# Performance work log

Measured on AMD Instinct MI355X. Metric: run time of the kernel, lower is better.

## Reference

```python
import jax, jax.numpy as jnp
import numpy as np

B, T, C = 4, 2048, 2048
N_HEAD, N_HEAD_KV = 16, 4
HEAD_DIM = C // N_HEAD
ROPE_BASE = 10000.0


def setup_inputs() -> dict:
    key = jax.random.key(0)
    ks = jax.random.split(key, 6)
    x = jax.random.normal(ks[0], (B, T, C), dtype=jnp.float32)
    # freqs_cis: (T, head_dim//2, 2) with [...,0]=cos, [...,1]=sin (true RoPE angles)
    inv_freq = 1.0 / (ROPE_BASE ** (jnp.arange(0, HEAD_DIM, 2, dtype=jnp.float32) / HEAD_DIM))
    angles = jnp.arange(T, dtype=jnp.float32)[:, None] * inv_freq[None, :]  # (T, hd//2)
    freqs_cis = jnp.stack([jnp.cos(angles), jnp.sin(angles)], axis=-1)
    s = 0.02
    Wq = jax.random.normal(ks[1], (C, C), dtype=jnp.float32) * s
    Wk = jax.random.normal(ks[2], (N_HEAD_KV * HEAD_DIM, C), dtype=jnp.float32) * s
    Wv = jax.random.normal(ks[3], (N_HEAD_KV * HEAD_DIM, C), dtype=jnp.float32) * s
    Wo = jax.random.normal(ks[4], (C, C), dtype=jnp.float32) * s
    return {"x": x, "freqs_cis": freqs_cis, "Wq": Wq, "Wk": Wk, "Wv": Wv, "Wo": Wo}


def _rotate_half(u):
    h = u.shape[-1] // 2
    return jnp.concatenate([-u[..., h:], u[..., :h]], axis=-1)


def reference(x, freqs_cis, Wq, Wk, Wv, Wo):
    b, t, c = x.shape
    hd = HEAD_DIM
    q = (x @ Wq.T).reshape(b, t, N_HEAD, hd)
    k = (x @ Wk.T).reshape(b, t, N_HEAD_KV, hd)
    v = (x @ Wv.T).reshape(b, t, N_HEAD_KV, hd)
    # external RoPE (3-dim freqs_cis): cos/sin repeated to full head_dim
    cos = freqs_cis[:t, :, 0]
    sin = freqs_cis[:t, :, 1]
    cos = jnp.concatenate([cos, cos], axis=-1)[None, :, None, :]  # (1,T,1,hd)
    sin = jnp.concatenate([sin, sin], axis=-1)[None, :, None, :]
    q = q * cos + _rotate_half(q) * sin
    k = k * cos + _rotate_half(k) * sin
    # GQA: repeat_interleave kv heads to n_head
    g = N_HEAD // N_HEAD_KV
    k = jnp.repeat(k, g, axis=2)  # (B,T,H,hd)
    v = jnp.repeat(v, g, axis=2)
    scale = 1.0 / np.sqrt(hd)
    scores = jnp.einsum('bthd,bshd->bhts', q, k) * scale  # (B,H,T,S)
    causal = jnp.tril(jnp.ones((t, t), dtype=bool))
    neg = jnp.finfo(scores.dtype).min
    scores = jnp.where(causal[None, None, :, :], scores, neg)
    attn = jax.nn.softmax(scores, axis=-1)
    out = jnp.einsum('bhts,bshd->bthd', attn, v).reshape(b, t, c)
    return out @ Wo.T
```

## Files before the change

### kernel.cpp

```cpp
#include <hip/hip_runtime.h>
#include <hip/hip_bf16.h>
#include <stdint.h>

typedef __bf16 bf16_t;
typedef __bf16 bf16x4 __attribute__((ext_vector_type(4)));
typedef __bf16 bf16x8 __attribute__((ext_vector_type(8)));
typedef float f32x4 __attribute__((ext_vector_type(4)));

__device__ __forceinline__ float fast_exp2(float x) {
#if __has_builtin(__builtin_amdgcn_exp2f)
  return __builtin_amdgcn_exp2f(x);
#else
  return exp2f(x);
#endif
}

__global__ void cvt_all(const float* __restrict__ x,  const float* __restrict__ Wq,
                        const float* __restrict__ Wk, const float* __restrict__ Wv,
                        const float* __restrict__ Wo, bf16_t* __restrict__ xb,
                        bf16_t* __restrict__ wqkv, bf16_t* __restrict__ wob) {
  const int bid = blockIdx.x, tid = threadIdx.x;
  const float* src; bf16_t* dst; int i;
  if (bid < 16384)      { src = x;  dst = xb;             i = bid * 256 + tid; }
  else if (bid < 20480) { src = Wq; dst = wqkv;           i = (bid - 16384) * 256 + tid; }
  else if (bid < 21504) { src = Wk; dst = wqkv + 4194304; i = (bid - 20480) * 256 + tid; }
  else if (bid < 22528) { src = Wv; dst = wqkv + 5242880; i = (bid - 21504) * 256 + tid; }
  else                  { src = Wo; dst = wob;            i = (bid - 22528) * 256 + tid; }
  float4 v = ((const float4*)src)[i];
  bf16x4 o = { (bf16_t)v.x, (bf16_t)v.y, (bf16_t)v.z, (bf16_t)v.w };
  *(bf16x4*)(dst + (size_t)i * 4) = o;
}

__device__ __forceinline__ void async_load16(const bf16_t* g, bf16_t* l) {
#if __has_builtin(__builtin_amdgcn_global_load_lds)
  __builtin_amdgcn_global_load_lds((const __attribute__((address_space(1))) void*)g,
                                   (__attribute__((address_space(3))) void*)l, 16, 0, 0);
#else
  *(bf16x8*)l = *(const bf16x8*)g;
#endif
}

template<bool F32OUT, bool VSPLIT>
__global__ __launch_bounds__(256) void gemm_bt(const bf16_t* __restrict__ A,
                                               const bf16_t* __restrict__ B,
                                               void* __restrict__ C,
                                               bf16_t* __restrict__ Vt,
                                               int M, int N, int K, int ldc) {
  __shared__ bf16_t Alds[128 * 64];
  __shared__ bf16_t Blds[128 * 64];
  const int tid = threadIdx.x;
  const int wave = tid >> 6, lane = tid & 63;
  const int lrow = lane & 15, quad = lane >> 4;
  const int wr = wave >> 1, wc = wave & 1;
  const int bm = blockIdx.y, bn = blockIdx.x;
  const bf16_t* Ab = A + (size_t)bm * 128 * K;
  const bf16_t* Bb = B + (size_t)bn * 128 * K;
  const int r0 = tid >> 3;
  const int c0 = ((tid & 7) ^ (r0 & 7)) << 3;
  f32x4 acc[4][4] = {};

  for (int kk = 0; kk < K; kk += 64) {
#pragma unroll
    for (int p = 0; p < 4; ++p) {
      async_load16(Ab + (size_t)(p * 32 + r0) * K + kk + c0, &Alds[(p * 256 + tid) * 8]);
      async_load16(Bb + (size_t)(p * 32 + r0) * K + kk + c0, &Blds[(p * 256 + tid) * 8]);
    }
    __syncthreads();
#pragma unroll
    for (int ks2 = 0; ks2 < 2; ++ks2) {
      const int rc = ((ks2 * 4 + quad) ^ (lrow & 7)) << 3;
      bf16x8 af[4], bfv[4];
#pragma unroll
      for (int mt = 0; mt < 4; ++mt)
        af[mt] = *(const bf16x8*)&Alds[(wr * 64 + mt * 16 + lrow) * 64 + rc];
#pragma unroll
      for (int nt = 0; nt < 4; ++nt)
        bfv[nt] = *(const bf16x8*)&Blds[(wc * 64 + nt * 16 + lrow) * 64 + rc];
#pragma unroll
      for (int mt = 0; mt < 4; ++mt)
#pragma unroll
        for (int nt = 0; nt < 4; ++nt)
          acc[mt][nt] = __builtin_amdgcn_mfma_f32_16x16x32_bf16(af[mt], bfv[nt], acc[mt][nt], 0, 0, 0);
    }
    __syncthreads();
  }

  if (VSPLIT && bn >= 20) {
#pragma unroll
    for (int mt = 0; mt < 4; ++mt)
#pragma unroll
      for (int nt = 0; nt < 4; ++nt) {
        int row = bm * 128 + wr * 64 + mt * 16 + quad * 4;
        int cv  = bn * 128 + wc * 64 + nt * 16 + lrow - 2560;
        int b = row >> 11, tl = row & 2047;
        bf16x4 o;
#pragma unroll
        for (int r = 0; r < 4; ++r) o[r] = (bf16_t)acc[mt][nt][r];
        *(bf16x4*)&Vt[((size_t)(b * 512 + cv)) * 2048 + tl] = o;
      }
    return;
  }
#pragma unroll
  for (int mt = 0; mt < 4; ++mt)
#pragma unroll
    for (int nt = 0; nt < 4; ++nt)
#pragma unroll
      for (int r = 0; r < 4; ++r) {
        int row = bm * 128 + wr * 64 + mt * 16 + quad * 4 + r;
        int col = bn * 128 + wc * 64 + nt * 16 + lrow;
        if (F32OUT) ((float*)C)[(size_t)row * ldc + col] = acc[mt][nt][r];
        else        ((bf16_t*)C)[(size_t)row * ldc + col] = (bf16_t)acc[mt][nt][r];
      }
}

__global__ void rope_kernel(bf16_t* __restrict__ X, const float* __restrict__ F,
                            int hshift, int stride) {
  int i = blockIdx.x * blockDim.x + threadIdx.x;
  int d = i & 63;
  int h = (i >> 6) & ((1 << hshift) - 1);
  int row = i >> (6 + hshift);
  int t = row & 2047;
  float c = F[t * 128 + d * 2];
  float s = F[t * 128 + d * 2 + 1];
  size_t base = (size_t)row * stride + h * 128 + d;
  float q0 = (float)X[base];
  float q1 = (float)X[base + 64];
  X[base]      = (bf16_t)(q0 * c - q1 * s);
  X[base + 64] = (bf16_t)(q1 * c + q0 * s);
}

__global__ __launch_bounds__(256, 2) void attn_kernel(const bf16_t* __restrict__ QKV,
                                                      const float* __restrict__ F,
                                                      const bf16_t* __restrict__ Vt,
                                                      bf16_t* __restrict__ O) {
  __shared__ bf16_t Ks[2][64 * 128];
  __shared__ bf16_t Vs[2][128 * 64];
  __shared__ bf16_t Ps[4 * 32 * 64];
  const int tid = threadIdx.x;
  const int wave = tid >> 6, lane = tid & 63;
  const int lrow = lane & 15, quad = lane >> 4;
  const int bh = blockIdx.y, b = bh >> 4, h = bh & 15, kvh = h >> 2;
  const size_t qoff  = ((size_t)b * 2048) * 2560 + (size_t)h * 128;
  const size_t koff  = ((size_t)b * 2048) * 2560 + 2048 + (size_t)kvh * 128;
  const size_t vtoff = ((size_t)(b * 4 + kvh) * 128) * 2048;
  const float qsc = 0.08838834764831845f * 1.44269504088896340736f;
  bf16_t* Pw = Ps + wave * (32 * 64);
  const float2* F2 = (const float2*)F;

  const int krow_l = tid >> 4;
  const int kdc    = (tid & 15) ^ (krow_l & 7);
  const int vrow_l = tid >> 3;
  const int vkc    = (tid & 7) ^ (vrow_l & 7);

  auto stage = [&](int kt, int bsel) {
    const bf16_t* Kg = QKV + koff + (size_t)(kt * 64) * 2560;
    const bf16_t* Vg = Vt + vtoff + kt * 64;
    bf16_t* Kd = &Ks[bsel][0];
    bf16_t* Vd = &Vs[bsel][0];
#pragma unroll
    for (int c4 = 0; c4 < 4; ++c4) {
      int ci = c4 * 256 + tid;
      async_load16(Kg + (size_t)(c4 * 16 + krow_l) * 2560 + kdc * 8, Kd + ci * 8);
      async_load16(Vg + (size_t)(c4 * 32 + vrow_l) * 2048 + vkc * 8, Vd + ci * 8);
    }
  };

  for (int phase = 0; phase < 2; ++phase) {
    const int qt = phase ? (15 - blockIdx.x) : blockIdx.x;
    const int qbase = qt * 128 + wave * 32;

    bf16x8 qf[2][4];
#pragma unroll
    for (int nt2 = 0; nt2 < 2; ++nt2) {
      const int t = qbase + nt2 * 16 + lrow;
      const bf16_t* qp = QKV + qoff + (size_t)t * 2560 + quad * 8;
      bf16x8 raw[4];
#pragma unroll
      for (int ks = 0; ks < 4; ++ks) raw[ks] = *(const bf16x8*)(qp + ks * 32);
#pragma unroll
      for (int ks2 = 0; ks2 < 2; ++ks2) {
        bf16x8 lo, hi;
#pragma unroll
        for (int j = 0; j < 8; ++j) {
          int d = ks2 * 32 + quad * 8 + j;
          float2 cs = F2[t * 64 + d];
          float q0 = (float)raw[ks2][j], q1 = (float)raw[ks2 + 2][j];
          lo[j] = (bf16_t)((q0 * cs.x - q1 * cs.y) * qsc);
          hi[j] = (bf16_t)((q1 * cs.x + q0 * cs.y) * qsc);
        }
        qf[nt2][ks2]     = lo;
        qf[nt2][ks2 + 2] = hi;
      }
    }

    f32x4 Oacc[2][8] = {};
    float m_r[2] = {-1.0e30f, -1.0e30f};
    float l_r[2] = {0.f, 0.f};
    const int kt_end = 2 * qt + 2;

    stage(0, 0);

    for (int kt = 0; kt < kt_end; ++kt) {
      __syncthreads();
      if (kt + 1 < kt_end) stage(kt + 1, (kt + 1) & 1);
      const bf16_t* Kb_ = &Ks[kt & 1][0];
      const bf16_t* Vb_ = &Vs[kt & 1][0];

      if (kt * 64 <= qbase + 31) {
        f32x4 S[2][4] = {};
#pragma unroll
        for (int ks = 0; ks < 4; ++ks) {
          bf16x8 kf[4];
#pragma unroll
          for (int mt = 0; mt < 4; ++mt) {
            int dc = (ks * 4 + quad) ^ (lrow & 7);
            kf[mt] = *(const bf16x8*)&Kb_[(mt * 16 + lrow) * 128 + dc * 8];
          }
          __builtin_amdgcn_s_setprio(1);
#pragma unroll
          for (int nt2 = 0; nt2 < 2; ++nt2)
#pragma unroll
            for (int mt = 0; mt < 4; ++mt)
              S[nt2][mt] = __builtin_amdgcn_mfma_f32_16x16x32_bf16(kf[mt], qf[nt2][ks], S[nt2][mt], 0, 0, 0);
          __builtin_amdgcn_s_setprio(0);
        }
        if (kt * 64 + 63 > qbase) {
#pragma unroll
          for (int nt2 = 0; nt2 < 2; ++nt2) {
            int q = qbase + nt2 * 16 + lrow;
#pragma unroll
            for (int mt = 0; mt < 4; ++mt) {
              int key0 = kt * 64 + mt * 16 + quad * 4;
#pragma unroll
              for (int r = 0; r < 4; ++r)
                if (key0 + r > q) S[nt2][mt][r] = -1.0e30f;
            }
          }
        }
        float alpha[2];
#pragma unroll
        for (int nt2 = 0; nt2 < 2; ++nt2) {
          float mx = -1.0e30f;
#pragma unroll
          for (int mt = 0; mt < 4; ++mt)
#pragma unroll
            for (int r = 0; r < 4; ++r) mx = fmaxf(mx, S[nt2][mt][r]);
          mx = fmaxf(mx, __shfl_xor(mx, 16, 64));
          mx = fmaxf(mx, __shfl_xor(mx, 32, 64));
          float mnew = fmaxf(m_r[nt2], mx);
          alpha[nt2] = fast_exp2(m_r[nt2] - mnew);
          m_r[nt2] = mnew;
          float rs = 0.f;
          const int prow = nt2 * 16 + lrow;
          const int pbase = prow * 64 + ((quad & 1) << 2);
#pragma unroll
          for (int mt = 0; mt < 4; ++mt) {
            bf16x4 pk;
#pragma unroll
            for (int r = 0; r < 4; ++r) {
              float p = fast_exp2(S[nt2][mt][r] - mnew);
              rs += p;
              pk[r] = (bf16_t)p;
            }
            int c8 = ((mt * 2 + (quad >> 1)) ^ (prow & 7)) << 3;
            *(bf16x4*)&Pw[pbase + c8] = pk;
          }
          rs += __shfl_xor(rs, 16, 64);
          rs += __shfl_xor(rs, 32, 64);
          l_r[nt2] = l_r[nt2] * alpha[nt2] + rs;
        }
        bool nz = (alpha[0] != 1.f) || (alpha[1] != 1.f);
        if (__ballot(nz) != 0ull) {
#pragma unroll
          for (int mt2 = 0; mt2 < 2; ++mt2)
#pragma unroll
            for (int r = 0; r < 4; ++r) {
              float av = __shfl(alpha[mt2], quad * 4 + r, 16);
#pragma unroll
              for (int dt = 0; dt < 8; ++dt) Oacc[mt2][dt][r] *= av;
            }
        }
#pragma unroll
        for (int ks2 = 0; ks2 < 2; ++ks2) {
          bf16x8 ap[2];
#pragma unroll
          for (int mt2 = 0; mt2 < 2; ++mt2) {
            int prow = mt2 * 16 + lrow;
            ap[mt2] = *(const bf16x8*)&Pw[prow * 64 + (((ks2 * 4 + quad) ^ (prow & 7)) << 3)];
          }
          int dc = (ks2 * 4 + quad) ^ (lrow & 7);
#pragma unroll
          for (int dt = 0; dt < 8; ++dt) {
            bf16x8 bv = *(const bf16x8*)&Vb_[(dt * 16 + lrow) * 64 + dc * 8];
            __builtin_amdgcn_s_setprio(1);
#pragma unroll
            for (int mt2 = 0; mt2 < 2; ++mt2)
              Oacc[mt2][dt] = __builtin_amdgcn_mfma_f32_16x16x32_bf16(ap[mt2], bv, Oacc[mt2][dt], 0, 0, 0);
            __builtin_amdgcn_s_setprio(0);
          }
        }
      }
    }

#pragma unroll
    for (int mt2 = 0; mt2 < 2; ++mt2)
#pragma unroll
      for (int r = 0; r < 4; ++r) {
        float lv = __shfl(l_r[mt2], quad * 4 + r, 16);
        float inv = 1.0f / lv;
        int row = qbase + mt2 * 16 + quad * 4 + r;
#pragma unroll
        for (int dt = 0; dt < 8; ++dt)
          O[(size_t)b * 2048 * 2048 + (size_t)row * 2048 + h * 128 + dt * 16 + lrow] =
              (bf16_t)(Oacc[mt2][dt][r] * inv);
      }
  }
}

extern "C" void kernel_launch(void* const* d_in, const int* in_sizes, int n_in,
                              void* d_out, int out_size, void* d_ws, size_t ws_size,
                              hipStream_t stream) {
  const float* x  = (const float*)d_in[0];
  const float* fc = (const float*)d_in[1];
  const float* Wq = (const float*)d_in[2];
  const float* Wk = (const float*)d_in[3];
  const float* Wv = (const float*)d_in[4];
  const float* Wo = (const float*)d_in[5];
  float* out = (float*)d_out;

  char* ws = (char*)d_ws;
  size_t off = 0;
  auto alloc = [&](size_t bytes) { char* p = ws + off; off += bytes; return p; };
  bf16_t* xb    = (bf16_t*)alloc((size_t)8192 * 2048 * 2);
  bf16_t* Wqkvb = (bf16_t*)alloc((size_t)3072 * 2048 * 2);
  bf16_t* Wob   = (bf16_t*)alloc((size_t)2048 * 2048 * 2);
  bf16_t* QKVb  = (bf16_t*)alloc((size_t)8192 * 2560 * 2);
  bf16_t* Ab    = (bf16_t*)alloc((size_t)8192 * 2048 * 2);
  bf16_t* Vtb   = (bf16_t*)alloc((size_t)2048 * 2048 * 2);
  (void)ws_size; (void)in_sizes; (void)n_in; (void)out_size;

  cvt_all<<<26624, 256, 0, stream>>>(x, Wq, Wk, Wv, Wo, xb, Wqkvb, Wob);

  gemm_bt<false, true><<<dim3(24, 64), 256, 0, stream>>>(xb, Wqkvb, QKVb, Vtb,
                                                         8192, 3072, 2048, 2560);

  rope_kernel<<<8192, 256, 0, stream>>>(QKVb + 2048, fc, 2, 2560);

  attn_kernel<<<dim3(8, 64), 256, 0, stream>>>(QKVb, fc, Vtb, Ab);

  gemm_bt<true, false><<<dim3(16, 64), 256, 0, stream>>>(Ab, Wob, out, nullptr,
                                                         8192, 2048, 2048, 2048);
}
```

Measured before the change: 472.6 us.

## Replace 128x128 GEMM with double-buffered 256x256 pipelined GEMM and remap workgroups

Replaces the 128x128-tile, single-buffered GEMM with a 512-thread, 256x256-tile kernel. It double-buffers LDS and splits each K step into four quadrant phases, so global prefetch of the next tile overlaps MFMA work through explicit vmcnt/lgkmcnt waits and barriers. Workgroup indices are remapped across XCD-style groups of eight to improve L2 locality. It also drops the s_setprio hints in the attention kernel. The bigger tiles need 128KB of LDS and many accumulator registers, which lowers occupancy, and the QKV GEMM launches only 384 workgroups.

```diff
diff --git a/kernel.cpp b/kernel.cpp
--- a/kernel.cpp
+++ b/kernel.cpp
@@ -41,76 +41,152 @@
 }
 
 template<bool F32OUT, bool VSPLIT>
-__global__ __launch_bounds__(256) void gemm_bt(const bf16_t* __restrict__ A,
-                                               const bf16_t* __restrict__ B,
-                                               void* __restrict__ C,
-                                               bf16_t* __restrict__ Vt,
-                                               int M, int N, int K, int ldc) {
-  __shared__ bf16_t Alds[128 * 64];
-  __shared__ bf16_t Blds[128 * 64];
+__global__ __launch_bounds__(512, 2) void gemm256(const bf16_t* __restrict__ A,
+                                                  const bf16_t* __restrict__ B,
+                                                  void* __restrict__ C,
+                                                  bf16_t* __restrict__ Vt,
+                                                  int NBN, int K, int ldc) {
+  __shared__ bf16_t As[2][256 * 64];
+  __shared__ bf16_t Bs[2][256 * 64];
   const int tid = threadIdx.x;
   const int wave = tid >> 6, lane = tid & 63;
   const int lrow = lane & 15, quad = lane >> 4;
-  const int wr = wave >> 1, wc = wave & 1;
-  const int bm = blockIdx.y, bn = blockIdx.x;
-  const bf16_t* Ab = A + (size_t)bm * 128 * K;
-  const bf16_t* Bb = B + (size_t)bn * 128 * K;
-  const int r0 = tid >> 3;
-  const int c0 = ((tid & 7) ^ (r0 & 7)) << 3;
-  f32x4 acc[4][4] = {};
-
-  for (int kk = 0; kk < K; kk += 64) {
-#pragma unroll
-    for (int p = 0; p < 4; ++p) {
-      async_load16(Ab + (size_t)(p * 32 + r0) * K + kk + c0, &Alds[(p * 256 + tid) * 8]);
-      async_load16(Bb + (size_t)(p * 32 + r0) * K + kk + c0, &Blds[(p * 256 + tid) * 8]);
-    }
-    __syncthreads();
-#pragma unroll
-    for (int ks2 = 0; ks2 < 2; ++ks2) {
-      const int rc = ((ks2 * 4 + quad) ^ (lrow & 7)) << 3;
-      bf16x8 af[4], bfv[4];
-#pragma unroll
-      for (int mt = 0; mt < 4; ++mt)
-        af[mt] = *(const bf16x8*)&Alds[(wr * 64 + mt * 16 + lrow) * 64 + rc];
-#pragma unroll
-      for (int nt = 0; nt < 4; ++nt)
-        bfv[nt] = *(const bf16x8*)&Blds[(wc * 64 + nt * 16 + lrow) * 64 + rc];
-#pragma unroll
-      for (int mt = 0; mt < 4; ++mt)
-#pragma unroll
-        for (int nt = 0; nt < 4; ++nt)
-          acc[mt][nt] = __builtin_amdgcn_mfma_f32_16x16x32_bf16(af[mt], bfv[nt], acc[mt][nt], 0, 0, 0);
-    }
-    __syncthreads();
+  const int wr = wave >> 2, wc = wave & 3;
+  const int nwg = gridDim.x;
+  const int wg  = (blockIdx.x & 7) * (nwg >> 3) + (blockIdx.x >> 3);
+  const int bm = wg / NBN, bn = wg % NBN;
+  const bf16_t* Ag = A + (size_t)bm * 256 * K;
+  const bf16_t* Bg = B + (size_t)bn * 256 * K;
+  const int srow = tid >> 3;
+  const int schunk = (tid & 7) ^ (srow & 7);
+
+  f32x4 acc[2][2][4][2] = {};
+  bf16x8 af[4][2], bfr[2][2];
+  const int NT = K >> 6;
+
+  auto stageA = [&](int mh, int bsel, int kk) {
+#pragma unroll
+    for (int i = 0; i < 2; ++i)
+      async_load16(Ag + (size_t)(mh * 128 + i * 64 + srow) * K + kk + schunk * 8,
+                   &As[bsel][mh * 8192 + i * 4096 + tid * 8]);
+  };
+  auto stageB = [&](int nh, int bsel, int kk) {
+#pragma unroll
+    for (int i = 0; i < 2; ++i)
+      async_load16(Bg + (size_t)(nh * 128 + i * 64 + srow) * K + kk + schunk * 8,
+                   &Bs[bsel][nh * 8192 + i * 4096 + tid * 8]);
+  };
+
+#define READ_A(MH)                                                                   \
+  _Pragma("unroll")                                                                  \
+  for (int mfi = 0; mfi < 4; ++mfi) {                                                \
+    const int ra = (MH) * 128 + mfi * 32 + wr * 16 + lrow;                           \
+    _Pragma("unroll")                                                                \
+    for (int ks = 0; ks < 2; ++ks)                                                   \
+      af[mfi][ks] = *(const bf16x8*)&As[buf][ra * 64 +                               \
+                        (((ks * 4 + quad) ^ (lrow & 7)) << 3)];                      \
   }
-
-  if (VSPLIT && bn >= 20) {
-#pragma unroll
-    for (int mt = 0; mt < 4; ++mt)
-#pragma unroll
-      for (int nt = 0; nt < 4; ++nt) {
-        int row = bm * 128 + wr * 64 + mt * 16 + quad * 4;
-        int cv  = bn * 128 + wc * 64 + nt * 16 + lrow - 2560;
-        int b = row >> 11, tl = row & 2047;
-        bf16x4 o;
-#pragma unroll
-        for (int r = 0; r < 4; ++r) o[r] = (bf16_t)acc[mt][nt][r];
-        *(bf16x4*)&Vt[((size_t)(b * 512 + cv)) * 2048 + tl] = o;
-      }
+#define READ_B(NH)                                                                   \
+  _Pragma("unroll")                                                                  \
+  for (int nfi = 0; nfi < 2; ++nfi) {                                                \
+    const int rb = (NH) * 128 + nfi * 64 + wc * 16 + lrow;                           \
+    _Pragma("unroll")                                                                \
+    for (int ks = 0; ks < 2; ++ks)                                                   \
+      bfr[nfi][ks] = *(const bf16x8*)&Bs[buf][rb * 64 +                              \
+                         (((ks * 4 + quad) ^ (lrow & 7)) << 3)];                     \
+  }
+#define MFMA_Q(MH, NH)                                                               \
+  __builtin_amdgcn_s_setprio(1);                                                     \
+  _Pragma("unroll")                                                                  \
+  for (int ks = 0; ks < 2; ++ks)                                                     \
+    _Pragma("unroll")                                                                \
+    for (int mfi = 0; mfi < 4; ++mfi)                                                \
+      _Pragma("unroll")                                                              \
+      for (int nfi = 0; nfi < 2; ++nfi)                                              \
+        acc[MH][NH][mfi][nfi] = __builtin_amdgcn_mfma_f32_16x16x32_bf16(             \
+            af[mfi][ks], bfr[nfi][ks], acc[MH][NH][mfi][nfi], 0, 0, 0);              \
+  __builtin_amdgcn_s_setprio(0);
+
+  stageA(0, 0, 0);
+  stageB(0, 0, 0);
+  stageB(1, 0, 0);
+  stageA(1, 0, 0);
+  asm volatile("s_waitcnt vmcnt(4)" ::: "memory");
+  __builtin_amdgcn_s_barrier();
+
+  for (int t = 0; t < NT; ++t) {
+    const int buf = t & 1, obuf = buf ^ 1;
+    const int kn = (t + 1) << 6;
+    const bool pf = (t + 1 < NT);
+    READ_A(0)
+    READ_B(0)
+    if (pf) stageA(0, obuf, kn);
+    __builtin_amdgcn_s_barrier();
+    asm volatile("s_waitcnt lgkmcnt(0)" ::: "memory");
+    MFMA_Q(0, 0)
+    if (pf) asm volatile("s_waitcnt vmcnt(4)" ::: "memory");
+    else    asm volatile("s_waitcnt vmcnt(2)" ::: "memory");
+    __builtin_amdgcn_s_barrier();
+    READ_B(1)
+    if (pf) stageB(0, obuf, kn);
+    __builtin_amdgcn_s_barrier();
+    asm volatile("s_waitcnt lgkmcnt(0)" ::: "memory");
+    MFMA_Q(0, 1)
+    if (pf) asm volatile("s_waitcnt vmcnt(4)" ::: "memory");
+    else    asm volatile("s_waitcnt vmcnt(0)" ::: "memory");
+    __builtin_amdgcn_s_barrier();
+    READ_A(1)
+    if (pf) stageB(1, obuf, kn);
+    __builtin_amdgcn_s_barrier();
+    asm volatile("s_waitcnt lgkmcnt(0)" ::: "memory");
+    MFMA_Q(1, 1)
+    __builtin_amdgcn_s_barrier();
+    READ_B(0)
+    if (pf) stageA(1, obuf, kn);
+    __builtin_amdgcn_s_barrier();
+    asm volatile("s_waitcnt lgkmcnt(0)" ::: "memory");
+    MFMA_Q(1, 0)
+    if (pf) asm volatile("s_waitcnt vmcnt(4)" ::: "memory");
+    __builtin_amdgcn_s_barrier();
+  }
+#undef READ_A
+#undef READ_B
+#undef MFMA_Q
+
+  if (VSPLIT && bn >= 10) {
+#pragma unroll
+    for (int mh = 0; mh < 2; ++mh)
+#pragma unroll
+      for (int nh = 0; nh < 2; ++nh)
+#pragma unroll
+        for (int mfi = 0; mfi < 4; ++mfi)
+#pragma unroll
+          for (int nfi = 0; nfi < 2; ++nfi) {
+            int row = bm * 256 + mh * 128 + mfi * 32 + wr * 16 + quad * 4;
+            int cv  = bn * 256 + nh * 128 + nfi * 64 + wc * 16 + lrow - 2560;
+            int b = row >> 11, tl = row & 2047;
+            bf16x4 o;
+#pragma unroll
+            for (int r = 0; r < 4; ++r) o[r] = (bf16_t)acc[mh][nh][mfi][nfi][r];
+            *(bf16x4*)&Vt[((size_t)(b * 512 + cv)) * 2048 + tl] = o;
+          }
     return;
   }
 #pragma unroll
-  for (int mt = 0; mt < 4; ++mt)
-#pragma unroll
-    for (int nt = 0; nt < 4; ++nt)
-#pragma unroll
-      for (int r = 0; r < 4; ++r) {
-        int row = bm * 128 + wr * 64 + mt * 16 + quad * 4 + r;
-        int col = bn * 128 + wc * 64 + nt * 16 + lrow;
-        if (F32OUT) ((float*)C)[(size_t)row * ldc + col] = acc[mt][nt][r];
-        else        ((bf16_t*)C)[(size_t)row * ldc + col] = (bf16_t)acc[mt][nt][r];
-      }
+  for (int mh = 0; mh < 2; ++mh)
+#pragma unroll
+    for (int nh = 0; nh < 2; ++nh)
+#pragma unroll
+      for (int mfi = 0; mfi < 4; ++mfi)
+#pragma unroll
+        for (int nfi = 0; nfi < 2; ++nfi)
+#pragma unroll
+          for (int r = 0; r < 4; ++r) {
+            int row = bm * 256 + mh * 128 + mfi * 32 + wr * 16 + quad * 4 + r;
+            int col = bn * 256 + nh * 128 + nfi * 64 + wc * 16 + lrow;
+            if (F32OUT) ((float*)C)[(size_t)row * ldc + col] = acc[mh][nh][mfi][nfi][r];
+            else        ((bf16_t*)C)[(size_t)row * ldc + col] = (bf16_t)acc[mh][nh][mfi][nfi][r];
+          }
 }
 
 __global__ void rope_kernel(bf16_t* __restrict__ X, const float* __restrict__ F,
@@ -216,13 +292,11 @@
             int dc = (ks * 4 + quad) ^ (lrow & 7);
             kf[mt] = *(const bf16x8*)&Kb_[(mt * 16 + lrow) * 128 + dc * 8];
           }
-          __builtin_amdgcn_s_setprio(1);
 #pragma unroll
           for (int nt2 = 0; nt2 < 2; ++nt2)
 #pragma unroll
             for (int mt = 0; mt < 4; ++mt)
               S[nt2][mt] = __builtin_amdgcn_mfma_f32_16x16x32_bf16(kf[mt], qf[nt2][ks], S[nt2][mt], 0, 0, 0);
-          __builtin_amdgcn_s_setprio(0);
         }
         if (kt * 64 + 63 > qbase) {
 #pragma unroll
@@ -292,11 +366,9 @@
 #pragma unroll
           for (int dt = 0; dt < 8; ++dt) {
             bf16x8 bv = *(const bf16x8*)&Vb_[(dt * 16 + lrow) * 64 + dc * 8];
-            __builtin_amdgcn_s_setprio(1);
 #pragma unroll
             for (int mt2 = 0; mt2 < 2; ++mt2)
               Oacc[mt2][dt] = __builtin_amdgcn_mfma_f32_16x16x32_bf16(ap[mt2], bv, Oacc[mt2][dt], 0, 0, 0);
-            __builtin_amdgcn_s_setprio(0);
           }
         }
       }
@@ -341,13 +413,11 @@
 
   cvt_all<<<26624, 256, 0, stream>>>(x, Wq, Wk, Wv, Wo, xb, Wqkvb, Wob);
 
-  gemm_bt<false, true><<<dim3(24, 64), 256, 0, stream>>>(xb, Wqkvb, QKVb, Vtb,
-                                                         8192, 3072, 2048, 2560);
+  gemm256<false, true><<<384, 512, 0, stream>>>(xb, Wqkvb, QKVb, Vtb, 12, 2048, 2560);
 
   rope_kernel<<<8192, 256, 0, stream>>>(QKVb + 2048, fc, 2, 2560);
 
   attn_kernel<<<dim3(8, 64), 256, 0, stream>>>(QKVb, fc, Vtb, Ab);
 
-  gemm_bt<true, false><<<dim3(16, 64), 256, 0, stream>>>(Ab, Wob, out, nullptr,
-                                                         8192, 2048, 2048, 2048);
-}
+  gemm256<true, false><<<256, 512, 0, stream>>>(Ab, Wob, out, nullptr, 8, 2048, 2048);
+}
```

Measured after the change: 463.2 us. 2.0% less time.
